# Kernel tuning notes

Hardware: AMD Instinct MI355X
Metric: run time of the kernel (lower is better)

The kernel has to match this reference:

```python
import jax, jax.numpy as jnp
import numpy as np

N_SAMPLES = 2048
BURN_IN = 128
STEP_SIZE = 0.1
D = 512   # walker dimension
H = 1024  # wavefunction MLP hidden width


def setup_inputs() -> dict:
    key = jax.random.key(0)
    k0, k1, k2 = jax.random.split(key, 3)
    x0 = jax.random.normal(k0, (1, D), dtype=jnp.float32)
    W1 = jax.random.normal(k1, (D, H), dtype=jnp.float32) / np.float32(np.sqrt(D))
    b1 = jnp.zeros((H,), dtype=jnp.float32)
    W2 = jax.random.normal(k2, (H, 1), dtype=jnp.float32) / np.float32(np.sqrt(H))
    b2 = jnp.zeros((1,), dtype=jnp.float32)
    return {"x0": x0, "W1": W1, "b1": b1, "W2": W2, "b2": b2}


def _model(x, W1, b1, W2, b2):
    # wavefunction MLP: [1, D] -> [1, 1]
    return jnp.tanh(x @ W1 + b1) @ W2 + b2


def reference(x0, W1, b1, W2, b2):
    def psi2(x):
        # model(x).pow(2)[0] -> shape [1]
        return (_model(x, W1, b1, W2, b2) ** 2)[0]

    def mh_step(x, k):
        k_noise, k_unif = jax.random.split(k)
        x_new = x + jax.random.normal(k_noise, x.shape, dtype=x.dtype) * STEP_SIZE
        p_new = psi2(x_new)
        p_old = psi2(x)
        ratio = jnp.minimum(p_new / (p_old + 1e-12), 1.0)          # clamp(max=1.0)
        u = jax.random.uniform(k_unif, ratio.shape, dtype=x.dtype)
        accept = (u < ratio).astype(x.dtype)[:, None]               # [1, 1]
        x = accept * x_new + (1.0 - accept) * x
        return x, x[0]  # carry chain state, record sample row [D]

    keys = jax.random.split(jax.random.key(1), N_SAMPLES + BURN_IN)
    _, traj = jax.lax.scan(mh_step, x0, keys)   # traj: [N+BURN_IN, D]
    return traj[BURN_IN:]                        # [N_SAMPLES, D]
```

## Files before the change

kernel.cpp:

```cpp
#include <hip/hip_runtime.h>
#include <stdint.h>
#include <math.h>


#define T_TOTAL 2176
#define NITER   1088
#define NROWS   2177
#define NBURN   128
#define DDIM    512
#define HDIM    1024
#define DONE_FLAG 0x13572468u

__device__ __forceinline__ uint2 tf2x32(uint32_t k0, uint32_t k1,
                                        uint32_t x0, uint32_t x1) {
  uint32_t ks2 = k0 ^ k1 ^ 0x1BD11BDAu;
  x0 += k0; x1 += k1;
#define TF_R(r) { x0 += x1; x1 = (x1 << (r)) | (x1 >> (32 - (r))); x1 ^= x0; }
  TF_R(13) TF_R(15) TF_R(26) TF_R(6)
  x0 += k1;  x1 += ks2 + 1u;
  TF_R(17) TF_R(29) TF_R(16) TF_R(24)
  x0 += ks2; x1 += k0 + 2u;
  TF_R(13) TF_R(15) TF_R(26) TF_R(6)
  x0 += k0;  x1 += k1 + 3u;
  TF_R(17) TF_R(29) TF_R(16) TF_R(24)
  x0 += k1;  x1 += ks2 + 4u;
  TF_R(13) TF_R(15) TF_R(26) TF_R(6)
  x0 += ks2; x1 += k0 + 5u;
#undef TF_R
  return make_uint2(x0, x1);
}

__device__ __forceinline__ float erfinv_xla(float x) {
  float w = -log1pf(-x * x);
  float p;
  if (w < 5.0f) {
    w = w - 2.5f;
    p = 2.81022636e-08f;
    p = fmaf(p, w, 3.43273939e-07f);
    p = fmaf(p, w, -3.5233877e-06f);
    p = fmaf(p, w, -4.39150654e-06f);
    p = fmaf(p, w, 0.00021858087f);
    p = fmaf(p, w, -0.00125372503f);
    p = fmaf(p, w, -0.00417768164f);
    p = fmaf(p, w, 0.246640727f);
    p = fmaf(p, w, 1.50140941f);
  } else {
    w = sqrtf(w) - 3.0f;
    p = -0.000200214257f;
    p = fmaf(p, w, 0.000100950558f);
    p = fmaf(p, w, 0.00134934322f);
    p = fmaf(p, w, -0.00367342844f);
    p = fmaf(p, w, 0.00573950773f);
    p = fmaf(p, w, -0.0076224613f);
    p = fmaf(p, w, 0.00943887047f);
    p = fmaf(p, w, 1.00167406f);
    p = fmaf(p, w, 2.83297682f);
  }
  return p * x;
}

__device__ __forceinline__ float normal_from_bits(uint32_t bits) {
  const float lo = -0.99999994f;
  float u01 = __uint_as_float(0x3f800000u | (bits >> 9)) - 1.0f;
  float v = u01 * 2.0f + lo;
  v = fmaxf(lo, v);
  return 1.41421356237309515f * erfinv_xla(v);
}

__device__ __forceinline__ float tanh_fast(float x) {
  float a = x * 2.88539008177792681472f;
#if __has_builtin(__builtin_amdgcn_exp2f)
  float e = __builtin_amdgcn_exp2f(a);
#else
  float e = exp2f(a);
#endif
  float r = __builtin_amdgcn_rcpf(e + 1.0f);
  return fmaf(-2.0f, r, 1.0f);
}

__global__ void __launch_bounds__(256) rng_kernel(const float* __restrict__ x0,
                                                  float* __restrict__ A,
                                                  double* __restrict__ A64,
                                                  float* __restrict__ U) {
  const uint32_t t = blockIdx.x;
  const int tid = threadIdx.x;
  uint2 kt = tf2x32(0u, 1u, 0u, t);
  uint2 kn = tf2x32(kt.x, kt.y, 0u, 0u);
  uint2 e0 = tf2x32(kn.x, kn.y, 0u, (uint32_t)tid);
  uint2 e1 = tf2x32(kn.x, kn.y, 0u, (uint32_t)(tid + 256));
  float n0 = normal_from_bits(e0.x ^ e0.y) * 0.1f;
  float n1 = normal_from_bits(e1.x ^ e1.y) * 0.1f;
  float* Arow = A + (size_t)(t + 1) * DDIM;
  Arow[tid]       = n0;
  Arow[tid + 256] = n1;
  if (A64) {
    double* Arow64 = A64 + (size_t)(t + 1) * DDIM;
    Arow64[tid]       = (double)n0;
    Arow64[tid + 256] = (double)n1;
  }
  if (tid == 0) {
    uint2 ku = tf2x32(kt.x, kt.y, 0u, 1u);
    uint2 eu = tf2x32(ku.x, ku.y, 0u, 0u);
    U[t] = __uint_as_float(0x3f800000u | ((eu.x ^ eu.y) >> 9)) - 1.0f;
  }
  if (t == 0) {
    float xv0 = x0[tid], xv1 = x0[tid + 256];
    A[tid]       = xv0;
    A[tid + 256] = xv1;
    if (A64) {
      A64[tid]       = (double)xv0;
      A64[tid + 256] = (double)xv1;
    }
  }
}

__global__ void __launch_bounds__(512) gemm64_kernel(
    const double* __restrict__ A64, const float* __restrict__ W1,
    float* __restrict__ Z, int nrows) {
  const int r0 = blockIdx.x * 4;
  const int t  = threadIdx.x;
  const int c0 = t, c1 = t + 512;
  double acc[4][2];
#pragma unroll
  for (int r = 0; r < 4; ++r) { acc[r][0] = 0.0; acc[r][1] = 0.0; }
  for (int d = 0; d < 512; d += 4) {
    double wA[4], wB[4];
#pragma unroll
    for (int j = 0; j < 4; ++j) {
      wA[j] = (double)W1[(size_t)(d + j) * 1024 + c0];
      wB[j] = (double)W1[(size_t)(d + j) * 1024 + c1];
    }
#pragma unroll
    for (int r = 0; r < 4; ++r) {
      int rr = r0 + r; if (rr >= nrows) rr = nrows - 1;
      const double2 a01 = *(const double2*)(A64 + (size_t)rr * 512 + d);
      const double2 a23 = *(const double2*)(A64 + (size_t)rr * 512 + d + 2);
      acc[r][0] += (a01.x * wA[0] + a01.y * wA[1]) +
                   (a23.x * wA[2] + a23.y * wA[3]);
      acc[r][1] += (a01.x * wB[0] + a01.y * wB[1]) +
                   (a23.x * wB[2] + a23.y * wB[3]);
    }
  }
  const int rmax = (nrows - r0 < 4) ? (nrows - r0) : 4;
  for (int r = 0; r < rmax; ++r) {
    Z[(size_t)(r0 + r) * 1024 + c0] = (float)acc[r][0];
    Z[(size_t)(r0 + r) * 1024 + c1] = (float)acc[r][1];
  }
}

__global__ void __launch_bounds__(512) gemm_kernel(const float* __restrict__ A,
                                                   const float* __restrict__ W1,
                                                   float* __restrict__ Z,
                                                   int nrows) {
  const int r0 = blockIdx.x * 4;
  const int t  = threadIdx.x;
  const int c0 = t, c1 = t + 512;
  double acc[4][2];
#pragma unroll
  for (int r = 0; r < 4; ++r) { acc[r][0] = 0.0; acc[r][1] = 0.0; }
  for (int d = 0; d < 512; d += 4) {
    double wA[4], wB[4];
#pragma unroll
    for (int j = 0; j < 4; ++j) {
      wA[j] = (double)W1[(size_t)(d + j) * 1024 + c0];
      wB[j] = (double)W1[(size_t)(d + j) * 1024 + c1];
    }
#pragma unroll
    for (int r = 0; r < 4; ++r) {
      int rr = r0 + r; if (rr >= nrows) rr = nrows - 1;
      const float4 a4 = *(const float4*)(A + (size_t)rr * 512 + d);
      double a0 = (double)a4.x, a1 = (double)a4.y;
      double a2 = (double)a4.z, a3 = (double)a4.w;
      acc[r][0] += (a0 * wA[0] + a1 * wA[1]) + (a2 * wA[2] + a3 * wA[3]);
      acc[r][1] += (a0 * wB[0] + a1 * wB[1]) + (a2 * wB[2] + a3 * wB[3]);
    }
  }
  const int rmax = (nrows - r0 < 4) ? (nrows - r0) : 4;
  for (int r = 0; r < rmax; ++r) {
    Z[(size_t)(r0 + r) * 1024 + c0] = (float)acc[r][0];
    Z[(size_t)(r0 + r) * 1024 + c1] = (float)acc[r][1];
  }
}

#define DPP_ADD(v, ctrl)                                                     \
  v += __int_as_float(__builtin_amdgcn_update_dpp(                           \
      0, __float_as_int(v), (ctrl), 0xF, 0xF, true))

__device__ __forceinline__ float wave_reduce_to_last(float v) {
  DPP_ADD(v, 0xB1);
  DPP_ADD(v, 0x4E);
  DPP_ADD(v, 0x141);
  DPP_ADD(v, 0x140);
  DPP_ADD(v, 0x142);
  DPP_ADD(v, 0x143);
  return v;
}

#define BAR() asm volatile("s_waitcnt lgkmcnt(0)\n\ts_barrier" ::: "memory")

__global__ void __launch_bounds__(256) chain_kernel(
    const float* __restrict__ Z, const float* __restrict__ A,
    const float* __restrict__ U, const float* __restrict__ x0,
    const float* __restrict__ b1, const float* __restrict__ W2,
    const float* __restrict__ b2, float* __restrict__ out,
    unsigned* __restrict__ flag) {
  const int tid = threadIdx.x;

  if (blockIdx.x != 0) {
    float acc = (float)tid * 1.0e-6f;
    for (int i = 0; i < 4000; ++i) {
#pragma unroll
      for (int jj = 0; jj < 256; ++jj) acc = fmaf(acc, 0.99999988f, 1.0e-7f);
      unsigned f = __hip_atomic_load(flag, __ATOMIC_RELAXED,
                                     __HIP_MEMORY_SCOPE_AGENT);
      if (f == DONE_FLAG) break;
    }
    if (acc == 123456.75f && tid == 1023) out[0] = acc;
    return;
  }

  const int lane = tid & 63;
  const int wid = tid >> 6;
  __shared__ __align__(16) float wsum[2][3][4];
  __shared__ float Uld[2184];

  const float4* Zv = (const float4*)Z;
  const float2* Av = (const float2*)A;

  for (int i = tid; i < 2184; i += 256) Uld[i] = U[i];

  const float4 w2v = ((const float4*)W2)[tid];
  const float4 b1v = ((const float4*)b1)[tid];
  const float b2v = b2[0];

  float4 z0r = Zv[tid];
  float4 z1r = Zv[256 + tid];
  float4 z2r = Zv[512 + tid];
  float4 zA0 = Zv[3 * 256 + tid], zB0 = Zv[4 * 256 + tid];
  float4 zA1 = Zv[5 * 256 + tid], zB1 = Zv[6 * 256 + tid];
  float2 dAa0 = Av[1 * 256 + tid], dAb0 = Av[2 * 256 + tid];
  float2 dAa1 = Av[3 * 256 + tid], dAb1 = Av[4 * 256 + tid];

  double Y0 = (double)z0r.x + (double)b1v.x;
  double Y1 = (double)z0r.y + (double)b1v.y;
  double Y2 = (double)z0r.z + (double)b1v.z;
  double Y3 = (double)z0r.w + (double)b1v.w;

  float xa = x0[2 * tid], xb = x0[2 * tid + 1];

  __syncthreads();

  {
    float g0 = tanh_fast((float)Y0);
    float g1 = tanh_fast((float)Y1);
    float g2 = tanh_fast((float)Y2);
    float g3 = tanh_fast((float)Y3);
    float tm = fmaf(g3, w2v.w, fmaf(g2, w2v.z, fmaf(g1, w2v.y, g0 * w2v.x)));
    tm = wave_reduce_to_last(tm);
    if (lane == 63) wsum[1][0][wid] = tm;
  }
  __syncthreads();
  float p;
  {
    const float4 pp = *(const float4*)wsum[1][0];
    float m0 = ((pp.x + pp.y) + (pp.z + pp.w)) + b2v;
    p = m0 * m0;
  }
  float um1 = Uld[0] * (p + 1e-12f);
  float u2c = Uld[1];

  double Ya0 = Y0 + (double)z1r.x, Ya1 = Y1 + (double)z1r.y;
  double Ya2 = Y2 + (double)z1r.z, Ya3 = Y3 + (double)z1r.w;
  double Yb0 = Y0 + (double)z2r.x, Yb1 = Y1 + (double)z2r.y;
  double Yb2 = Y2 + (double)z2r.z, Yb3 = Y3 + (double)z2r.w;
  double Yc0 = Ya0 + (double)z2r.x, Yc1 = Ya1 + (double)z2r.y;
  double Yc2 = Ya2 + (double)z2r.z, Yc3 = Ya3 + (double)z2r.w;
  {
    float a0 = tanh_fast((float)Ya0), a1 = tanh_fast((float)Ya1);
    float a2 = tanh_fast((float)Ya2), a3 = tanh_fast((float)Ya3);
    float b0 = tanh_fast((float)Yb0), b1_ = tanh_fast((float)Yb1);
    float b2_ = tanh_fast((float)Yb2), b3 = tanh_fast((float)Yb3);
    float c0 = tanh_fast((float)Yc0), c1 = tanh_fast((float)Yc1);
    float c2 = tanh_fast((float)Yc2), c3 = tanh_fast((float)Yc3);
    float tA = fmaf(a3, w2v.w, fmaf(a2, w2v.z, fmaf(a1, w2v.y, a0 * w2v.x)));
    float tB = fmaf(b3, w2v.w, fmaf(b2_, w2v.z, fmaf(b1_, w2v.y, b0 * w2v.x)));
    float tC = fmaf(c3, w2v.w, fmaf(c2, w2v.z, fmaf(c1, w2v.y, c0 * w2v.x)));
    tA = wave_reduce_to_last(tA);
    tB = wave_reduce_to_last(tB);
    tC = wave_reduce_to_last(tC);
    if (lane == 63) {
      wsum[0][0][wid] = tA;
      wsum[0][1][wid] = tB;
      wsum[0][2][wid] = tC;
    }
  }
  __syncthreads();

#define ITER(k, PAR, ZAB, ZBB, DAB, DBB)                                     \
  {                                                                          \
    float u1n = Uld[2 * (k) + 2];                                            \
    float u2n = Uld[2 * (k) + 3];                                            \
    const float4 e1 = *(const float4*)wsum[PAR][0];                          \
    const float4 e2 = *(const float4*)wsum[PAR][1];                          \
    const float4 e3 = *(const float4*)wsum[PAR][2];                          \
    float m1 = ((e1.x + e1.y) + (e1.z + e1.w)) + b2v;                        \
    float q1 = m1 * m1;                                                      \
    bool a1v = um1 < q1;                                                     \
    float p1 = a1v ? q1 : p;                                                 \
    float um2 = u2c * (p1 + 1e-12f);                                         \
    float m2v = ((e2.x + e2.y) + (e2.z + e2.w)) + b2v;                       \
    float m3v = ((e3.x + e3.y) + (e3.z + e3.w)) + b2v;                       \
    float m23 = a1v ? m3v : m2v;                                             \
    float q23 = m23 * m23;                                                   \
    bool a2v = um2 < q23;                                                    \
    p = a2v ? q23 : p1;                                                      \
    float xat = a1v ? xa + DAB.x : xa;                                       \
    float xbt = a1v ? xb + DAB.y : xb;                                       \
    xa = a2v ? xat + DBB.x : xat;                                            \
    xb = a2v ? xbt + DBB.y : xbt;                                            \
    if ((k) >= 64) {                                                         \
      float2 o1; o1.x = xat; o1.y = xbt;                                     \
      *(float2*)(out + (size_t)(2 * (k) - NBURN) * DDIM + 2 * tid) = o1;     \
      float2 o2; o2.x = xa; o2.y = xb;                                       \
      *(float2*)(out + (size_t)(2 * (k) + 1 - NBURN) * DDIM + 2 * tid) = o2; \
    }                                                                        \
    DAB = Av[(size_t)(2 * (k) + 5) * 256 + tid];                             \
    DBB = Av[(size_t)(2 * (k) + 6) * 256 + tid];                             \
    Y0 = a1v ? (a2v ? Yc0 : Ya0) : (a2v ? Yb0 : Y0);                         \
    Y1 = a1v ? (a2v ? Yc1 : Ya1) : (a2v ? Yb1 : Y1);                         \
    Y2 = a1v ? (a2v ? Yc2 : Ya2) : (a2v ? Yb2 : Y2);                         \
    Y3 = a1v ? (a2v ? Yc3 : Ya3) : (a2v ? Yb3 : Y3);                         \
    Ya0 = Y0 + (double)ZAB.x;  Ya1 = Y1 + (double)ZAB.y;                     \
    Ya2 = Y2 + (double)ZAB.z;  Ya3 = Y3 + (double)ZAB.w;                     \
    Yb0 = Y0 + (double)ZBB.x;  Yb1 = Y1 + (double)ZBB.y;                     \
    Yb2 = Y2 + (double)ZBB.z;  Yb3 = Y3 + (double)ZBB.w;                     \
    Yc0 = Ya0 + (double)ZBB.x; Yc1 = Ya1 + (double)ZBB.y;                    \
    Yc2 = Ya2 + (double)ZBB.z; Yc3 = Ya3 + (double)ZBB.w;                    \
    ZAB = Zv[(size_t)(2 * (k) + 7) * 256 + tid];                             \
    ZBB = Zv[(size_t)(2 * (k) + 8) * 256 + tid];                             \
    float ga0 = tanh_fast((float)Ya0), ga1 = tanh_fast((float)Ya1);          \
    float ga2 = tanh_fast((float)Ya2), ga3 = tanh_fast((float)Ya3);          \
    float gb0 = tanh_fast((float)Yb0), gb1 = tanh_fast((float)Yb1);          \
    float gb2 = tanh_fast((float)Yb2), gb3 = tanh_fast((float)Yb3);          \
    float gc0 = tanh_fast((float)Yc0), gc1 = tanh_fast((float)Yc1);          \
    float gc2 = tanh_fast((float)Yc2), gc3 = tanh_fast((float)Yc3);          \
    float tA = fmaf(ga3, w2v.w, fmaf(ga2, w2v.z, fmaf(ga1, w2v.y, ga0 * w2v.x))); \
    float tB = fmaf(gb3, w2v.w, fmaf(gb2, w2v.z, fmaf(gb1, w2v.y, gb0 * w2v.x))); \
    float tC = fmaf(gc3, w2v.w, fmaf(gc2, w2v.z, fmaf(gc1, w2v.y, gc0 * w2v.x))); \
    tA = wave_reduce_to_last(tA);                                            \
    tB = wave_reduce_to_last(tB);                                            \
    tC = wave_reduce_to_last(tC);                                            \
    if (lane == 63) {                                                        \
      wsum[(PAR) ^ 1][0][wid] = tA;                                          \
      wsum[(PAR) ^ 1][1][wid] = tB;                                          \
      wsum[(PAR) ^ 1][2][wid] = tC;                                          \
    }                                                                        \
    um1 = u1n * (p + 1e-12f);                                                \
    u2c = u2n;                                                               \
    BAR();                                                                   \
  }

  for (int k = 0; k < NITER; k += 2) {
    ITER(k,     0, zA0, zB0, dAa0, dAb0);
    ITER(k + 1, 1, zA1, zB1, dAa1, dAb1);
  }
#undef ITER

  if (tid == 0) {
    __hip_atomic_store(flag, DONE_FLAG, __ATOMIC_RELAXED,
                       __HIP_MEMORY_SCOPE_AGENT);
  }
}

extern "C" void kernel_launch(void* const* d_in, const int* in_sizes, int n_in,
                              void* d_out, int out_size, void* d_ws, size_t ws_size,
                              hipStream_t stream) {
  const float* x0 = (const float*)d_in[0];
  const float* W1 = (const float*)d_in[1];
  const float* b1 = (const float*)d_in[2];
  const float* W2 = (const float*)d_in[3];
  const float* b2 = (const float*)d_in[4];
  float* out = (float*)d_out;

  char* ws = (char*)d_ws;
  float* A = (float*)ws;
  float* Z = (float*)(ws + 4472832);
  float* U = (float*)(ws + 4472832 + 8945664);
  unsigned* flag = (unsigned*)(ws + 4472832 + 8945664 + 8736);
  size_t a64_off = 13427328;
  double* A64 = (double*)(ws + a64_off);
  bool use64 = (ws_size >= a64_off + (size_t)2184 * 512 * 8);

  rng_kernel<<<T_TOTAL, 256, 0, stream>>>(x0, A, use64 ? A64 : (double*)nullptr, U);
  if (use64)
    gemm64_kernel<<<546, 512, 0, stream>>>(A64, W1, Z, NROWS);
  else
    gemm_kernel<<<546, 512, 0, stream>>>(A, W1, Z, NROWS);
  chain_kernel<<<256, 256, 0, stream>>>(Z, A, U, x0, b1, W2, b2, out, flag);
}
```

Baseline: 816.6 us.

## Resolve three MH steps per barrier via speculative evaluation of all outcomes

Widens speculative lookahead from two to three Metropolis steps per block barrier. Each round evaluates the model for all seven possible accept/reject paths over the next three proposals, then resolves them serially. This cuts the barrier count by about a third. In exchange each round does more tanh and reduction work (seven candidates instead of three) and holds more registers.

```diff
diff --git a/kernel.cpp b/kernel.cpp
--- a/kernel.cpp
+++ b/kernel.cpp
@@ -4,7 +4,6 @@
 
 
 #define T_TOTAL 2176
-#define NITER   1088
 #define NROWS   2177
 #define NBURN   128
 #define DDIM    512
@@ -196,6 +195,13 @@
   return v;
 }
 
+__device__ __forceinline__ float psidot(double q0, double q1, double q2,
+                                        double q3, float4 w2v) {
+  float g0 = tanh_fast((float)q0), g1 = tanh_fast((float)q1);
+  float g2 = tanh_fast((float)q2), g3 = tanh_fast((float)q3);
+  return fmaf(g3, w2v.w, fmaf(g2, w2v.z, fmaf(g1, w2v.y, g0 * w2v.x)));
+}
+
 #define BAR() asm volatile("s_waitcnt lgkmcnt(0)\n\ts_barrier" ::: "memory")
 
 __global__ void __launch_bounds__(256) chain_kernel(
@@ -221,7 +227,7 @@
 
   const int lane = tid & 63;
   const int wid = tid >> 6;
-  __shared__ __align__(16) float wsum[2][3][4];
+  __shared__ __align__(16) float wsum[2][7][4];
   __shared__ float Uld[2184];
 
   const float4* Zv = (const float4*)Z;
@@ -234,12 +240,10 @@
   const float b2v = b2[0];
 
   float4 z0r = Zv[tid];
-  float4 z1r = Zv[256 + tid];
-  float4 z2r = Zv[512 + tid];
-  float4 zA0 = Zv[3 * 256 + tid], zB0 = Zv[4 * 256 + tid];
-  float4 zA1 = Zv[5 * 256 + tid], zB1 = Zv[6 * 256 + tid];
-  float2 dAa0 = Av[1 * 256 + tid], dAb0 = Av[2 * 256 + tid];
-  float2 dAa1 = Av[3 * 256 + tid], dAb1 = Av[4 * 256 + tid];
+  float4 zA0 = Zv[1 * 256 + tid], zA1 = Zv[2 * 256 + tid], zA2 = Zv[3 * 256 + tid];
+  float4 zB0 = Zv[4 * 256 + tid], zB1 = Zv[5 * 256 + tid], zB2 = Zv[6 * 256 + tid];
+  float2 dA0 = Av[1 * 256 + tid], dA1 = Av[2 * 256 + tid], dA2 = Av[3 * 256 + tid];
+  float2 dB0 = Av[4 * 256 + tid], dB1 = Av[5 * 256 + tid], dB2 = Av[6 * 256 + tid];
 
   double Y0 = (double)z0r.x + (double)b1v.x;
   double Y1 = (double)z0r.y + (double)b1v.y;
@@ -251,11 +255,7 @@
   __syncthreads();
 
   {
-    float g0 = tanh_fast((float)Y0);
-    float g1 = tanh_fast((float)Y1);
-    float g2 = tanh_fast((float)Y2);
-    float g3 = tanh_fast((float)Y3);
-    float tm = fmaf(g3, w2v.w, fmaf(g2, w2v.z, fmaf(g1, w2v.y, g0 * w2v.x)));
+    float tm = psidot(Y0, Y1, Y2, Y3, w2v);
     tm = wave_reduce_to_last(tm);
     if (lane == 63) wsum[1][0][wid] = tm;
   }
@@ -267,104 +267,142 @@
     p = m0 * m0;
   }
   float um1 = Uld[0] * (p + 1e-12f);
-  float u2c = Uld[1];
-
-  double Ya0 = Y0 + (double)z1r.x, Ya1 = Y1 + (double)z1r.y;
-  double Ya2 = Y2 + (double)z1r.z, Ya3 = Y3 + (double)z1r.w;
-  double Yb0 = Y0 + (double)z2r.x, Yb1 = Y1 + (double)z2r.y;
-  double Yb2 = Y2 + (double)z2r.z, Yb3 = Y3 + (double)z2r.w;
-  double Yc0 = Ya0 + (double)z2r.x, Yc1 = Ya1 + (double)z2r.y;
-  double Yc2 = Ya2 + (double)z2r.z, Yc3 = Ya3 + (double)z2r.w;
-  {
-    float a0 = tanh_fast((float)Ya0), a1 = tanh_fast((float)Ya1);
-    float a2 = tanh_fast((float)Ya2), a3 = tanh_fast((float)Ya3);
-    float b0 = tanh_fast((float)Yb0), b1_ = tanh_fast((float)Yb1);
-    float b2_ = tanh_fast((float)Yb2), b3 = tanh_fast((float)Yb3);
-    float c0 = tanh_fast((float)Yc0), c1 = tanh_fast((float)Yc1);
-    float c2 = tanh_fast((float)Yc2), c3 = tanh_fast((float)Yc3);
-    float tA = fmaf(a3, w2v.w, fmaf(a2, w2v.z, fmaf(a1, w2v.y, a0 * w2v.x)));
-    float tB = fmaf(b3, w2v.w, fmaf(b2_, w2v.z, fmaf(b1_, w2v.y, b0 * w2v.x)));
-    float tC = fmaf(c3, w2v.w, fmaf(c2, w2v.z, fmaf(c1, w2v.y, c0 * w2v.x)));
-    tA = wave_reduce_to_last(tA);
-    tB = wave_reduce_to_last(tB);
-    tC = wave_reduce_to_last(tC);
-    if (lane == 63) {
-      wsum[0][0][wid] = tA;
-      wsum[0][1][wid] = tB;
-      wsum[0][2][wid] = tC;
-    }
-  }
+  float u2c = Uld[1], u3c = Uld[2];
+
+#define BUILD_EVAL(NXTBUF, ZN0, ZN1, ZN2)                                    \
+  {                                                                          \
+    double cA0 = Y0 + (double)(ZN0).x, cA1 = Y1 + (double)(ZN0).y,           \
+           cA2 = Y2 + (double)(ZN0).z, cA3 = Y3 + (double)(ZN0).w;           \
+    double cB0 = Y0 + (double)(ZN1).x, cB1 = Y1 + (double)(ZN1).y,           \
+           cB2 = Y2 + (double)(ZN1).z, cB3 = Y3 + (double)(ZN1).w;           \
+    double cC0 = cA0 + (double)(ZN1).x, cC1 = cA1 + (double)(ZN1).y,         \
+           cC2 = cA2 + (double)(ZN1).z, cC3 = cA3 + (double)(ZN1).w;         \
+    double cD0 = Y0 + (double)(ZN2).x, cD1 = Y1 + (double)(ZN2).y,           \
+           cD2 = Y2 + (double)(ZN2).z, cD3 = Y3 + (double)(ZN2).w;           \
+    double cE0 = cA0 + (double)(ZN2).x, cE1 = cA1 + (double)(ZN2).y,         \
+           cE2 = cA2 + (double)(ZN2).z, cE3 = cA3 + (double)(ZN2).w;         \
+    double cF0 = cB0 + (double)(ZN2).x, cF1 = cB1 + (double)(ZN2).y,         \
+           cF2 = cB2 + (double)(ZN2).z, cF3 = cB3 + (double)(ZN2).w;         \
+    double cG0 = cC0 + (double)(ZN2).x, cG1 = cC1 + (double)(ZN2).y,         \
+           cG2 = cC2 + (double)(ZN2).z, cG3 = cC3 + (double)(ZN2).w;         \
+    float tA = psidot(cA0, cA1, cA2, cA3, w2v);                              \
+    float tB = psidot(cB0, cB1, cB2, cB3, w2v);                              \
+    float tC = psidot(cC0, cC1, cC2, cC3, w2v);                              \
+    float tD = psidot(cD0, cD1, cD2, cD3, w2v);                              \
+    float tE = psidot(cE0, cE1, cE2, cE3, w2v);                              \
+    float tF = psidot(cF0, cF1, cF2, cF3, w2v);                              \
+    float tG = psidot(cG0, cG1, cG2, cG3, w2v);                              \
+    tA = wave_reduce_to_last(tA);                                            \
+    tB = wave_reduce_to_last(tB);                                            \
+    tC = wave_reduce_to_last(tC);                                            \
+    tD = wave_reduce_to_last(tD);                                            \
+    tE = wave_reduce_to_last(tE);                                            \
+    tF = wave_reduce_to_last(tF);                                            \
+    tG = wave_reduce_to_last(tG);                                            \
+    if (lane == 63) {                                                        \
+      wsum[NXTBUF][0][wid] = tA; wsum[NXTBUF][1][wid] = tB;                  \
+      wsum[NXTBUF][2][wid] = tC; wsum[NXTBUF][3][wid] = tD;                  \
+      wsum[NXTBUF][4][wid] = tE; wsum[NXTBUF][5][wid] = tF;                  \
+      wsum[NXTBUF][6][wid] = tG;                                             \
+    }                                                                        \
+  }
+
+  BUILD_EVAL(0, zA0, zA1, zA2)
   __syncthreads();
 
-#define ITER(k, PAR, ZAB, ZBB, DAB, DBB)                                     \
+#define ITER3(k, PAR, ZC0, ZC1, ZC2, DC0, DC1, DC2, ZN0, ZN1, ZN2)           \
   {                                                                          \
-    float u1n = Uld[2 * (k) + 2];                                            \
-    float u2n = Uld[2 * (k) + 3];                                            \
-    const float4 e1 = *(const float4*)wsum[PAR][0];                          \
-    const float4 e2 = *(const float4*)wsum[PAR][1];                          \
-    const float4 e3 = *(const float4*)wsum[PAR][2];                          \
-    float m1 = ((e1.x + e1.y) + (e1.z + e1.w)) + b2v;                        \
+    float u1n = Uld[3 * (k) + 3];                                            \
+    float u2n = Uld[3 * (k) + 4];                                            \
+    float u3n = Uld[3 * (k) + 5];                                            \
+    const float4 e0 = *(const float4*)wsum[PAR][0];                          \
+    const float4 e1 = *(const float4*)wsum[PAR][1];                          \
+    const float4 e2 = *(const float4*)wsum[PAR][2];                          \
+    const float4 e3 = *(const float4*)wsum[PAR][3];                          \
+    const float4 e4 = *(const float4*)wsum[PAR][4];                          \
+    const float4 e5 = *(const float4*)wsum[PAR][5];                          \
+    const float4 e6 = *(const float4*)wsum[PAR][6];                          \
+    float m1 = ((e0.x + e0.y) + (e0.z + e0.w)) + b2v;                        \
     float q1 = m1 * m1;                                                      \
     bool a1v = um1 < q1;                                                     \
     float p1 = a1v ? q1 : p;                                                 \
+    float mB = ((e1.x + e1.y) + (e1.z + e1.w)) + b2v;                        \
+    float mC = ((e2.x + e2.y) + (e2.z + e2.w)) + b2v;                        \
+    float m2s = a1v ? mC : mB;                                               \
+    float q2 = m2s * m2s;                                                    \
     float um2 = u2c * (p1 + 1e-12f);                                         \
-    float m2v = ((e2.x + e2.y) + (e2.z + e2.w)) + b2v;                       \
-    float m3v = ((e3.x + e3.y) + (e3.z + e3.w)) + b2v;                       \
-    float m23 = a1v ? m3v : m2v;                                             \
-    float q23 = m23 * m23;                                                   \
-    bool a2v = um2 < q23;                                                    \
-    p = a2v ? q23 : p1;                                                      \
-    float xat = a1v ? xa + DAB.x : xa;                                       \
-    float xbt = a1v ? xb + DAB.y : xb;                                       \
-    xa = a2v ? xat + DBB.x : xat;                                            \
-    xb = a2v ? xbt + DBB.y : xbt;                                            \
-    if ((k) >= 64) {                                                         \
-      float2 o1; o1.x = xat; o1.y = xbt;                                     \
-      *(float2*)(out + (size_t)(2 * (k) - NBURN) * DDIM + 2 * tid) = o1;     \
-      float2 o2; o2.x = xa; o2.y = xb;                                       \
-      *(float2*)(out + (size_t)(2 * (k) + 1 - NBURN) * DDIM + 2 * tid) = o2; \
+    bool a2v = um2 < q2;                                                     \
+    float p2 = a2v ? q2 : p1;                                                \
+    float mD = ((e3.x + e3.y) + (e3.z + e3.w)) + b2v;                        \
+    float mE = ((e4.x + e4.y) + (e4.z + e4.w)) + b2v;                        \
+    float mF = ((e5.x + e5.y) + (e5.z + e5.w)) + b2v;                        \
+    float mG = ((e6.x + e6.y) + (e6.z + e6.w)) + b2v;                        \
+    float m3s = a1v ? (a2v ? mG : mE) : (a2v ? mF : mD);                     \
+    float q3 = m3s * m3s;                                                    \
+    float um3 = u3c * (p2 + 1e-12f);                                         \
+    bool a3v = um3 < q3;                                                     \
+    p = a3v ? q3 : p2;                                                       \
+    float xa1 = a1v ? xa + (DC0).x : xa;                                     \
+    float xb1 = a1v ? xb + (DC0).y : xb;                                     \
+    float xa2 = a2v ? xa1 + (DC1).x : xa1;                                   \
+    float xb2 = a2v ? xb1 + (DC1).y : xb1;                                   \
+    xa = a3v ? xa2 + (DC2).x : xa2;                                          \
+    xb = a3v ? xb2 + (DC2).y : xb2;                                          \
+    if (3 * (k) + 1 >= NBURN + 1) {                                          \
+      float2 o; o.x = xa1; o.y = xb1;                                        \
+      *(float2*)(out + (size_t)(3 * (k) + 1 - (NBURN + 1)) * DDIM + 2 * tid) = o; \
     }                                                                        \
-    DAB = Av[(size_t)(2 * (k) + 5) * 256 + tid];                             \
-    DBB = Av[(size_t)(2 * (k) + 6) * 256 + tid];                             \
-    Y0 = a1v ? (a2v ? Yc0 : Ya0) : (a2v ? Yb0 : Y0);                         \
-    Y1 = a1v ? (a2v ? Yc1 : Ya1) : (a2v ? Yb1 : Y1);                         \
-    Y2 = a1v ? (a2v ? Yc2 : Ya2) : (a2v ? Yb2 : Y2);                         \
-    Y3 = a1v ? (a2v ? Yc3 : Ya3) : (a2v ? Yb3 : Y3);                         \
-    Ya0 = Y0 + (double)ZAB.x;  Ya1 = Y1 + (double)ZAB.y;                     \
-    Ya2 = Y2 + (double)ZAB.z;  Ya3 = Y3 + (double)ZAB.w;                     \
-    Yb0 = Y0 + (double)ZBB.x;  Yb1 = Y1 + (double)ZBB.y;                     \
-    Yb2 = Y2 + (double)ZBB.z;  Yb3 = Y3 + (double)ZBB.w;                     \
-    Yc0 = Ya0 + (double)ZBB.x; Yc1 = Ya1 + (double)ZBB.y;                    \
-    Yc2 = Ya2 + (double)ZBB.z; Yc3 = Ya3 + (double)ZBB.w;                    \
-    ZAB = Zv[(size_t)(2 * (k) + 7) * 256 + tid];                             \
-    ZBB = Zv[(size_t)(2 * (k) + 8) * 256 + tid];                             \
-    float ga0 = tanh_fast((float)Ya0), ga1 = tanh_fast((float)Ya1);          \
-    float ga2 = tanh_fast((float)Ya2), ga3 = tanh_fast((float)Ya3);          \
-    float gb0 = tanh_fast((float)Yb0), gb1 = tanh_fast((float)Yb1);          \
-    float gb2 = tanh_fast((float)Yb2), gb3 = tanh_fast((float)Yb3);          \
-    float gc0 = tanh_fast((float)Yc0), gc1 = tanh_fast((float)Yc1);          \
-    float gc2 = tanh_fast((float)Yc2), gc3 = tanh_fast((float)Yc3);          \
-    float tA = fmaf(ga3, w2v.w, fmaf(ga2, w2v.z, fmaf(ga1, w2v.y, ga0 * w2v.x))); \
-    float tB = fmaf(gb3, w2v.w, fmaf(gb2, w2v.z, fmaf(gb1, w2v.y, gb0 * w2v.x))); \
-    float tC = fmaf(gc3, w2v.w, fmaf(gc2, w2v.z, fmaf(gc1, w2v.y, gc0 * w2v.x))); \
-    tA = wave_reduce_to_last(tA);                                            \
-    tB = wave_reduce_to_last(tB);                                            \
-    tC = wave_reduce_to_last(tC);                                            \
-    if (lane == 63) {                                                        \
-      wsum[(PAR) ^ 1][0][wid] = tA;                                          \
-      wsum[(PAR) ^ 1][1][wid] = tB;                                          \
-      wsum[(PAR) ^ 1][2][wid] = tC;                                          \
+    if (3 * (k) + 2 >= NBURN + 1) {                                          \
+      float2 o; o.x = xa2; o.y = xb2;                                        \
+      *(float2*)(out + (size_t)(3 * (k) + 2 - (NBURN + 1)) * DDIM + 2 * tid) = o; \
     }                                                                        \
+    if (3 * (k) + 3 >= NBURN + 1) {                                          \
+      float2 o; o.x = xa; o.y = xb;                                          \
+      *(float2*)(out + (size_t)(3 * (k) + 3 - (NBURN + 1)) * DDIM + 2 * tid) = o; \
+    }                                                                        \
+    Y0 += (double)(a1v ? (ZC0).x : 0.0f);                                    \
+    Y1 += (double)(a1v ? (ZC0).y : 0.0f);                                    \
+    Y2 += (double)(a1v ? (ZC0).z : 0.0f);                                    \
+    Y3 += (double)(a1v ? (ZC0).w : 0.0f);                                    \
+    Y0 += (double)(a2v ? (ZC1).x : 0.0f);                                    \
+    Y1 += (double)(a2v ? (ZC1).y : 0.0f);                                    \
+    Y2 += (double)(a2v ? (ZC1).z : 0.0f);                                    \
+    Y3 += (double)(a2v ? (ZC1).w : 0.0f);                                    \
+    Y0 += (double)(a3v ? (ZC2).x : 0.0f);                                    \
+    Y1 += (double)(a3v ? (ZC2).y : 0.0f);                                    \
+    Y2 += (double)(a3v ? (ZC2).z : 0.0f);                                    \
+    Y3 += (double)(a3v ? (ZC2).w : 0.0f);                                    \
+    ZC0 = Zv[(size_t)(3 * (k) + 7) * 256 + tid];                             \
+    ZC1 = Zv[(size_t)(3 * (k) + 8) * 256 + tid];                             \
+    ZC2 = Zv[(size_t)(3 * (k) + 9) * 256 + tid];                             \
+    DC0 = Av[(size_t)(3 * (k) + 7) * 256 + tid];                             \
+    DC1 = Av[(size_t)(3 * (k) + 8) * 256 + tid];                             \
+    DC2 = Av[(size_t)(3 * (k) + 9) * 256 + tid];                             \
+    BUILD_EVAL((PAR) ^ 1, ZN0, ZN1, ZN2)                                     \
     um1 = u1n * (p + 1e-12f);                                                \
     u2c = u2n;                                                               \
+    u3c = u3n;                                                               \
     BAR();                                                                   \
   }
 
-  for (int k = 0; k < NITER; k += 2) {
-    ITER(k,     0, zA0, zB0, dAa0, dAb0);
-    ITER(k + 1, 1, zA1, zB1, dAa1, dAb1);
-  }
-#undef ITER
+  for (int k = 0; k < 724; k += 2) {
+    ITER3(k,     0, zA0, zA1, zA2, dA0, dA1, dA2, zB0, zB1, zB2);
+    ITER3(k + 1, 1, zB0, zB1, zB2, dB0, dB1, dB2, zA0, zA1, zA2);
+  }
+  ITER3(724, 0, zA0, zA1, zA2, dA0, dA1, dA2, zB0, zB1, zB2);
+#undef ITER3
+#undef BUILD_EVAL
+
+  {
+    const float4 pp = *(const float4*)wsum[1][0];
+    float m1 = ((pp.x + pp.y) + (pp.z + pp.w)) + b2v;
+    float q1 = m1 * m1;
+    bool a1v = um1 < q1;
+    float2 o;
+    o.x = a1v ? xa + dB0.x : xa;
+    o.y = a1v ? xb + dB0.y : xb;
+    *(float2*)(out + (size_t)(T_TOTAL - NBURN - 1) * DDIM + 2 * tid) = o;
+  }
 
   if (tid == 0) {
     __hip_atomic_store(flag, DONE_FLAG, __ATOMIC_RELAXED,
```

New measurement: 995.8 us. 1.22x slower.

## Split chain block into two thread groups evaluating candidate proposals in parallel

Applied to the files above, without the earlier changes.

Doubles the chain block to 512 threads. The first 256 threads evaluate the A candidate, track the walker state and write outputs, while the second 256 evaluate the B and C candidates, so each thread does fewer tanh evaluations per step. The goal is a shorter serial critical path per MH step. The cost is redundant Y updates and Z loads in both groups and a barrier that now spans 8 waves instead of 4.

```diff
diff --git a/kernel.cpp b/kernel.cpp
--- a/kernel.cpp
+++ b/kernel.cpp
@@ -196,9 +196,16 @@
   return v;
 }
 
+__device__ __forceinline__ float psidot(double q0, double q1, double q2,
+                                        double q3, float4 w2v) {
+  float g0 = tanh_fast((float)q0), g1 = tanh_fast((float)q1);
+  float g2 = tanh_fast((float)q2), g3 = tanh_fast((float)q3);
+  return fmaf(g3, w2v.w, fmaf(g2, w2v.z, fmaf(g1, w2v.y, g0 * w2v.x)));
+}
+
 #define BAR() asm volatile("s_waitcnt lgkmcnt(0)\n\ts_barrier" ::: "memory")
 
-__global__ void __launch_bounds__(256) chain_kernel(
+__global__ void __launch_bounds__(512) chain_kernel(
     const float* __restrict__ Z, const float* __restrict__ A,
     const float* __restrict__ U, const float* __restrict__ x0,
     const float* __restrict__ b1, const float* __restrict__ W2,
@@ -219,43 +226,45 @@
     return;
   }
 
+  const int t8   = tid & 255;
+  const int g    = tid >> 8;
   const int lane = tid & 63;
-  const int wid = tid >> 6;
+  const int wid  = tid >> 6;
   __shared__ __align__(16) float wsum[2][3][4];
   __shared__ float Uld[2184];
 
   const float4* Zv = (const float4*)Z;
   const float2* Av = (const float2*)A;
 
-  for (int i = tid; i < 2184; i += 256) Uld[i] = U[i];
-
-  const float4 w2v = ((const float4*)W2)[tid];
-  const float4 b1v = ((const float4*)b1)[tid];
+  for (int i = tid; i < 2184; i += 512) Uld[i] = U[i];
+
+  const float4 w2v = ((const float4*)W2)[t8];
+  const float4 b1v = ((const float4*)b1)[t8];
   const float b2v = b2[0];
 
-  float4 z0r = Zv[tid];
-  float4 z1r = Zv[256 + tid];
-  float4 z2r = Zv[512 + tid];
-  float4 zA0 = Zv[3 * 256 + tid], zB0 = Zv[4 * 256 + tid];
-  float4 zA1 = Zv[5 * 256 + tid], zB1 = Zv[6 * 256 + tid];
-  float2 dAa0 = Av[1 * 256 + tid], dAb0 = Av[2 * 256 + tid];
-  float2 dAa1 = Av[3 * 256 + tid], dAb1 = Av[4 * 256 + tid];
+  float4 z0r = Zv[t8];
+  float4 z1r = Zv[256 + t8];
+  float4 z2r = Zv[512 + t8];
+  float4 zA0 = Zv[3 * 256 + t8], zB0 = Zv[4 * 256 + t8];
+  float4 zA1 = Zv[5 * 256 + t8], zB1 = Zv[6 * 256 + t8];
+
+  float2 dAa0 = make_float2(0.f, 0.f), dAb0 = dAa0, dAa1 = dAa0, dAb1 = dAa0;
+  float xa = 0.f, xb = 0.f;
+  if (g == 0) {
+    dAa0 = Av[1 * 256 + t8]; dAb0 = Av[2 * 256 + t8];
+    dAa1 = Av[3 * 256 + t8]; dAb1 = Av[4 * 256 + t8];
+    xa = x0[2 * t8]; xb = x0[2 * t8 + 1];
+  }
 
   double Y0 = (double)z0r.x + (double)b1v.x;
   double Y1 = (double)z0r.y + (double)b1v.y;
   double Y2 = (double)z0r.z + (double)b1v.z;
   double Y3 = (double)z0r.w + (double)b1v.w;
 
-  float xa = x0[2 * tid], xb = x0[2 * tid + 1];
-
   __syncthreads();
 
-  {
-    float g0 = tanh_fast((float)Y0);
-    float g1 = tanh_fast((float)Y1);
-    float g2 = tanh_fast((float)Y2);
-    float g3 = tanh_fast((float)Y3);
-    float tm = fmaf(g3, w2v.w, fmaf(g2, w2v.z, fmaf(g1, w2v.y, g0 * w2v.x)));
+  if (g == 0) {
+    float tm = psidot(Y0, Y1, Y2, Y3, w2v);
     tm = wave_reduce_to_last(tm);
     if (lane == 63) wsum[1][0][wid] = tm;
   }
@@ -275,23 +284,18 @@
   double Yb2 = Y2 + (double)z2r.z, Yb3 = Y3 + (double)z2r.w;
   double Yc0 = Ya0 + (double)z2r.x, Yc1 = Ya1 + (double)z2r.y;
   double Yc2 = Ya2 + (double)z2r.z, Yc3 = Ya3 + (double)z2r.w;
-  {
-    float a0 = tanh_fast((float)Ya0), a1 = tanh_fast((float)Ya1);
-    float a2 = tanh_fast((float)Ya2), a3 = tanh_fast((float)Ya3);
-    float b0 = tanh_fast((float)Yb0), b1_ = tanh_fast((float)Yb1);
-    float b2_ = tanh_fast((float)Yb2), b3 = tanh_fast((float)Yb3);
-    float c0 = tanh_fast((float)Yc0), c1 = tanh_fast((float)Yc1);
-    float c2 = tanh_fast((float)Yc2), c3 = tanh_fast((float)Yc3);
-    float tA = fmaf(a3, w2v.w, fmaf(a2, w2v.z, fmaf(a1, w2v.y, a0 * w2v.x)));
-    float tB = fmaf(b3, w2v.w, fmaf(b2_, w2v.z, fmaf(b1_, w2v.y, b0 * w2v.x)));
-    float tC = fmaf(c3, w2v.w, fmaf(c2, w2v.z, fmaf(c1, w2v.y, c0 * w2v.x)));
+  if (g == 0) {
+    float tA = psidot(Ya0, Ya1, Ya2, Ya3, w2v);
     tA = wave_reduce_to_last(tA);
+    if (lane == 63) wsum[0][0][wid] = tA;
+  } else {
+    float tB = psidot(Yb0, Yb1, Yb2, Yb3, w2v);
+    float tC = psidot(Yc0, Yc1, Yc2, Yc3, w2v);
     tB = wave_reduce_to_last(tB);
     tC = wave_reduce_to_last(tC);
     if (lane == 63) {
-      wsum[0][0][wid] = tA;
-      wsum[0][1][wid] = tB;
-      wsum[0][2][wid] = tC;
+      wsum[0][1][wid & 3] = tB;
+      wsum[0][2][wid & 3] = tC;
     }
   }
   __syncthreads();
@@ -314,18 +318,20 @@
     float q23 = m23 * m23;                                                   \
     bool a2v = um2 < q23;                                                    \
     p = a2v ? q23 : p1;                                                      \
-    float xat = a1v ? xa + DAB.x : xa;                                       \
-    float xbt = a1v ? xb + DAB.y : xb;                                       \
-    xa = a2v ? xat + DBB.x : xat;                                            \
-    xb = a2v ? xbt + DBB.y : xbt;                                            \
-    if ((k) >= 64) {                                                         \
-      float2 o1; o1.x = xat; o1.y = xbt;                                     \
-      *(float2*)(out + (size_t)(2 * (k) - NBURN) * DDIM + 2 * tid) = o1;     \
-      float2 o2; o2.x = xa; o2.y = xb;                                       \
-      *(float2*)(out + (size_t)(2 * (k) + 1 - NBURN) * DDIM + 2 * tid) = o2; \
+    if (g == 0) {                                                            \
+      float xat = a1v ? xa + DAB.x : xa;                                     \
+      float xbt = a1v ? xb + DAB.y : xb;                                     \
+      xa = a2v ? xat + DBB.x : xat;                                          \
+      xb = a2v ? xbt + DBB.y : xbt;                                          \
+      if ((k) >= 64) {                                                       \
+        float2 o1; o1.x = xat; o1.y = xbt;                                   \
+        *(float2*)(out + (size_t)(2 * (k) - NBURN) * DDIM + 2 * t8) = o1;    \
+        float2 o2; o2.x = xa; o2.y = xb;                                     \
+        *(float2*)(out + (size_t)(2 * (k) + 1 - NBURN) * DDIM + 2 * t8) = o2;\
+      }                                                                      \
+      DAB = Av[(size_t)(2 * (k) + 5) * 256 + t8];                            \
+      DBB = Av[(size_t)(2 * (k) + 6) * 256 + t8];                            \
     }                                                                        \
-    DAB = Av[(size_t)(2 * (k) + 5) * 256 + tid];                             \
-    DBB = Av[(size_t)(2 * (k) + 6) * 256 + tid];                             \
     Y0 = a1v ? (a2v ? Yc0 : Ya0) : (a2v ? Yb0 : Y0);                         \
     Y1 = a1v ? (a2v ? Yc1 : Ya1) : (a2v ? Yb1 : Y1);                         \
     Y2 = a1v ? (a2v ? Yc2 : Ya2) : (a2v ? Yb2 : Y2);                         \
@@ -336,24 +342,21 @@
     Yb2 = Y2 + (double)ZBB.z;  Yb3 = Y3 + (double)ZBB.w;                     \
     Yc0 = Ya0 + (double)ZBB.x; Yc1 = Ya1 + (double)ZBB.y;                    \
     Yc2 = Ya2 + (double)ZBB.z; Yc3 = Ya3 + (double)ZBB.w;                    \
-    ZAB = Zv[(size_t)(2 * (k) + 7) * 256 + tid];                             \
-    ZBB = Zv[(size_t)(2 * (k) + 8) * 256 + tid];                             \
-    float ga0 = tanh_fast((float)Ya0), ga1 = tanh_fast((float)Ya1);          \
-    float ga2 = tanh_fast((float)Ya2), ga3 = tanh_fast((float)Ya3);          \
-    float gb0 = tanh_fast((float)Yb0), gb1 = tanh_fast((float)Yb1);          \
-    float gb2 = tanh_fast((float)Yb2), gb3 = tanh_fast((float)Yb3);          \
-    float gc0 = tanh_fast((float)Yc0), gc1 = tanh_fast((float)Yc1);          \
-    float gc2 = tanh_fast((float)Yc2), gc3 = tanh_fast((float)Yc3);          \
-    float tA = fmaf(ga3, w2v.w, fmaf(ga2, w2v.z, fmaf(ga1, w2v.y, ga0 * w2v.x))); \
-    float tB = fmaf(gb3, w2v.w, fmaf(gb2, w2v.z, fmaf(gb1, w2v.y, gb0 * w2v.x))); \
-    float tC = fmaf(gc3, w2v.w, fmaf(gc2, w2v.z, fmaf(gc1, w2v.y, gc0 * w2v.x))); \
-    tA = wave_reduce_to_last(tA);                                            \
-    tB = wave_reduce_to_last(tB);                                            \
-    tC = wave_reduce_to_last(tC);                                            \
-    if (lane == 63) {                                                        \
-      wsum[(PAR) ^ 1][0][wid] = tA;                                          \
-      wsum[(PAR) ^ 1][1][wid] = tB;                                          \
-      wsum[(PAR) ^ 1][2][wid] = tC;                                          \
+    ZAB = Zv[(size_t)(2 * (k) + 7) * 256 + t8];                              \
+    ZBB = Zv[(size_t)(2 * (k) + 8) * 256 + t8];                              \
+    if (g == 0) {                                                            \
+      float tA = psidot(Ya0, Ya1, Ya2, Ya3, w2v);                            \
+      tA = wave_reduce_to_last(tA);                                          \
+      if (lane == 63) wsum[(PAR) ^ 1][0][wid] = tA;                          \
+    } else {                                                                 \
+      float tB = psidot(Yb0, Yb1, Yb2, Yb3, w2v);                            \
+      float tC = psidot(Yc0, Yc1, Yc2, Yc3, w2v);                            \
+      tB = wave_reduce_to_last(tB);                                          \
+      tC = wave_reduce_to_last(tC);                                          \
+      if (lane == 63) {                                                      \
+        wsum[(PAR) ^ 1][1][wid & 3] = tB;                                    \
+        wsum[(PAR) ^ 1][2][wid & 3] = tC;                                    \
+      }                                                                      \
     }                                                                        \
     um1 = u1n * (p + 1e-12f);                                                \
     u2c = u2n;                                                               \
@@ -396,5 +399,5 @@
     gemm64_kernel<<<546, 512, 0, stream>>>(A64, W1, Z, NROWS);
   else
     gemm_kernel<<<546, 512, 0, stream>>>(A, W1, Z, NROWS);
-  chain_kernel<<<256, 256, 0, stream>>>(Z, A, U, x0, b1, W2, b2, out, flag);
-}
+  chain_kernel<<<256, 512, 0, stream>>>(Z, A, U, x0, b1, W2, b2, out, flag);
+}
```

Measured after the change: 952.9 us. 1.17x slower.
